# Kernel optimization log

Measured on AMD Instinct MI355X. Metric: run time of the kernel, lower is better.

Reference implementation:

```python
import jax, jax.numpy as jnp
import numpy as np

N_NODES = 100000
N_EDGES = 3200000
IN_DIM, HID, LAT = 81, 64, 32
BN_EPS = 1e-5


def setup_inputs() -> dict:
    key = jax.random.key(0)
    ks = jax.random.split(key, 16)
    def w(k, fan_in, fan_out):
        lim = 1.0 / np.sqrt(fan_in)
        return jax.random.uniform(k, (fan_in, fan_out), jnp.float32, -lim, lim)
    inp = {
        "x": jax.random.normal(ks[0], (N_NODES, IN_DIM), jnp.float32),
        "edge_index": jax.random.randint(ks[1], (2, N_EDGES), 0, N_NODES, jnp.int64),
        "W1": w(ks[2], IN_DIM, HID), "b1": jnp.zeros((HID,), jnp.float32),
        "g1": jnp.ones((HID,), jnp.float32), "beta1": jnp.zeros((HID,), jnp.float32),
        "W2": w(ks[3], HID, HID), "b2": jnp.zeros((HID,), jnp.float32),
        "g2": jnp.ones((HID,), jnp.float32), "beta2": jnp.zeros((HID,), jnp.float32),
        "Wmu": w(ks[4], HID, LAT), "bmu": jnp.zeros((LAT,), jnp.float32),
        "Wls": w(ks[5], HID, LAT), "bls": jnp.zeros((LAT,), jnp.float32),
    }
    return inp


def _gcn_norm(edge_index, num_nodes):
    # PyG gcn_norm: add self-loops, symmetric D^-1/2 A D^-1/2
    loop = jnp.arange(num_nodes, dtype=edge_index.dtype)
    src = jnp.concatenate([edge_index[0], loop])
    dst = jnp.concatenate([edge_index[1], loop])
    deg = jax.ops.segment_sum(jnp.ones_like(src, dtype=jnp.float32), dst,
                              num_segments=num_nodes)
    dis = jnp.where(deg > 0, jax.lax.rsqrt(jnp.maximum(deg, 1.0)), 0.0)
    norm = dis[src] * dis[dst]  # [E + N]
    return src, dst, norm


def _gcn_conv(x, W, b, src, dst, norm, num_nodes):
    h = x @ W                          # [N, out]
    msg = h[src] * norm[:, None]       # gather + scale
    out = jax.ops.segment_sum(msg, dst, num_segments=num_nodes)  # scatter-add
    return out + b


def _batchnorm(h, g, beta):
    m = h.mean(axis=0)
    v = h.var(axis=0)  # biased, as torch uses for normalization
    return (h - m) * jax.lax.rsqrt(v + BN_EPS) * g + beta


def reference(x, edge_index, W1, b1, g1, beta1, W2, b2, g2, beta2,
              Wmu, bmu, Wls, bls):
    n = x.shape[0]
    src, dst, norm = _gcn_norm(edge_index, n)
    h = _gcn_conv(x, W1, b1, src, dst, norm, n)
    h = jax.nn.relu(_batchnorm(h, g1, beta1))  # dropout = identity (eval)
    h = _gcn_conv(h, W2, b2, src, dst, norm, n)
    h = jax.nn.relu(_batchnorm(h, g2, beta2))
    mu = _gcn_conv(h, Wmu, bmu, src, dst, norm, n)
    logstd = _gcn_conv(h, Wls, bls, src, dst, norm, n)
    return (mu, logstd)
```

## Files before the change

### kernel.cpp

```cpp
#include <hip/hip_runtime.h>
#include <stdint.h>

#define N_NODES 100000
#define N_EDGES 3200000
#define IN_DIM  81
#define HID     64
#define LAT     32
#define BN_EPS  1e-5f
#define NBUCKET 391
#define EPB     8192
#define NBLK_E  391
#define BCAP    16384

__device__ __forceinline__ float bfu2f(unsigned short u) {
    return __uint_as_float(((uint32_t)u) << 16);
}
__device__ __forceinline__ unsigned short f2bfu(float f) {
    uint32_t x = __float_as_uint(f);
    return (unsigned short)((x + 0x7FFFu + ((x >> 16) & 1u)) >> 16);
}
__device__ __forceinline__ float loadf(const void* p, size_t i, int fp32) {
    if (fp32) return ((const float*)p)[i];
    return bfu2f(((const unsigned short*)p)[i]);
}
__device__ __forceinline__ int load_dst(const void* ei, int f64, long e) {
    if (f64) return (int)(((const long long*)ei)[(size_t)N_EDGES + e]);
    return ((const int*)ei)[(size_t)N_EDGES + e];
}
__device__ __forceinline__ int load_src(const void* ei, int f64, long e) {
    if (f64) return (int)(((const long long*)ei)[e]);
    return ((const int*)ei)[e];
}
__device__ __forceinline__ float bcast(float v, int k) {
    return __int_as_float(__builtin_amdgcn_readlane(__float_as_int(v), k));
}

__device__ __forceinline__ void fma8(float* acc, uint4 v, float d) {
    acc[0] = fmaf(__uint_as_float(v.x << 16), d, acc[0]);
    acc[1] = fmaf(__uint_as_float(v.x & 0xffff0000u), d, acc[1]);
    acc[2] = fmaf(__uint_as_float(v.y << 16), d, acc[2]);
    acc[3] = fmaf(__uint_as_float(v.y & 0xffff0000u), d, acc[3]);
    acc[4] = fmaf(__uint_as_float(v.z << 16), d, acc[4]);
    acc[5] = fmaf(__uint_as_float(v.z & 0xffff0000u), d, acc[5]);
    acc[6] = fmaf(__uint_as_float(v.w << 16), d, acc[6]);
    acc[7] = fmaf(__uint_as_float(v.w & 0xffff0000u), d, acc[7]);
}

__global__ void stamp_kernel(float* out, int n, float v) {
    int i = blockIdx.x * blockDim.x + threadIdx.x;
    if (i < n) out[i] = v;
}

__global__ void detect_all(const int* ei_raw,
                           const void* x, const void* W1, const void* b1,
                           const void* g1, const void* be1, const void* W2,
                           const void* b2, const void* g2, const void* be2,
                           const void* Wmu, const void* bmu, const void* Wls,
                           const void* bls, int* flags,
                           float* statsA, float* statsB, int* gcnt) {
    int w = threadIdx.x >> 6;
    int lane = threadIdx.x & 63;
    if (w == 14) {
        for (int i = lane; i < 128; i += 64) statsA[i] = 0.0f;
        return;
    }
    if (w == 15) {
        for (int i = lane; i < 128; i += 64) statsB[i] = 0.0f;
        return;
    }
    if (w == 13) {
        int acc = ei_raw[2 * lane * 11003 + 1] |
                  ei_raw[2 * (lane + 64) * 11003 + 1];
        unsigned long long b = __ballot(acc != 0);
        if (lane == 0) flags[0] = (b == 0ull) ? 1 : 0;
        for (int i = lane; i < NBUCKET; i += 64) gcnt[i] = 0;
        return;
    }
    const void* bufs[13] = { x, W1, b1, g1, be1, W2, b2, g2, be2, Wmu, bmu, Wls, bls };
    const int   ns[13]   = { 512, 512, 64, 64, 64, 512, 64, 64, 64, 512, 32, 512, 32 };
    const unsigned short* u = (const unsigned short*)bufs[w];
    int n = ns[w];
    int evenZero = 0;
    bool oddNz = false, anyNz = false, big = false;
    for (int i = lane; i < n; i += 64) {
        unsigned short s = u[i];
        if (s) anyNz = true;
        if (i & 1) { if (s) oddNz = true; }
        else {
            if ((s & 0x7F80u) == 0x7F80u) big = true;
            else if (fabsf(bfu2f(s)) > 100.0f) big = true;
            if (s == 0) evenZero++;
        }
    }
    unsigned long long anyB = __ballot(anyNz);
    unsigned long long oddB = __ballot(oddNz);
    unsigned long long bigB = __ballot(big);
#pragma unroll
    for (int o = 1; o < 64; o <<= 1) evenZero += __shfl_xor(evenZero, o);
    if (lane == 0) {
        int fp32 = 0;
        if (anyB != 0ull) {
            if (bigB != 0ull) fp32 = 1;
            else if (evenZero >= n / 4 && oddB != 0ull) fp32 = 1;
        }
        flags[1 + w] = fp32;
    }
}

__global__ void convert_weights(const void* W1, const void* W2,
                                const void* Wmu, const void* Wls,
                                const void* b1, const void* b2,
                                const void* bmu, const void* bls,
                                const int* flags,
                                float* W1f, float* W2f, float* Wcatf,
                                float* b1f, float* b2f, float* bcatf) {
    int i = blockIdx.x * blockDim.x + threadIdx.x;
    if (i < IN_DIM * HID) { W1f[i] = loadf(W1, i, flags[2]); return; }
    i -= IN_DIM * HID;
    if (i < HID * HID) { W2f[i] = loadf(W2, i, flags[6]); return; }
    i -= HID * HID;
    if (i < HID * HID) {
        int k = i >> 6;
        int j = i & 63;
        if (j < LAT) Wcatf[i] = loadf(Wmu, (size_t)k * LAT + j, flags[10]);
        else         Wcatf[i] = loadf(Wls, (size_t)k * LAT + (j - LAT), flags[12]);
        return;
    }
    i -= HID * HID;
    if (i < HID) { b1f[i] = loadf(b1, i, flags[3]); return; }
    i -= HID;
    if (i < HID) { b2f[i] = loadf(b2, i, flags[7]); return; }
    i -= HID;
    if (i < HID) {
        if (i < LAT) bcatf[i] = loadf(bmu, i, flags[11]);
        else         bcatf[i] = loadf(bls, i - LAT, flags[13]);
    }
}

__global__ void bucket_scatter(const void* ei, const int* flags, int* gcnt,
                               int* staged) {
    __shared__ int h[NBUCKET];
    __shared__ int lbase[NBUCKET];
    __shared__ int lcnt[NBUCKET];
    for (int i = threadIdx.x; i < NBUCKET; i += 256) { h[i] = 0; lcnt[i] = 0; }
    __syncthreads();
    int f64 = flags[0];
    long e0 = (long)blockIdx.x * EPB;
    for (int i = 0; i < EPB / 256; i++) {
        long e = e0 + i * 256 + threadIdx.x;
        if (e < N_EDGES) atomicAdd(&h[load_dst(ei, f64, e) >> 8], 1);
    }
    __syncthreads();
    for (int i = threadIdx.x; i < NBUCKET; i += 256)
        lbase[i] = h[i] ? atomicAdd(&gcnt[i], h[i]) : 0;
    __syncthreads();
    for (int i = 0; i < EPB / 256; i++) {
        long e = e0 + i * 256 + threadIdx.x;
        if (e < N_EDGES) {
            int d = load_dst(ei, f64, e);
            int s = load_src(ei, f64, e);
            int b = d >> 8;
            int off = atomicAdd(&lcnt[b], 1);
            staged[(b << 14) + lbase[b] + off] = ((d & 255) << 17) | s;
        }
    }
}

__global__ void csr_build(const int* gcnt, const int* staged, float* dis,
                          int* row_start, int* csr) {
    int b = blockIdx.x;
    int t = threadIdx.x;
    int n0 = b << 8;
    int nn = N_NODES - n0;
    if (nn > 256) nn = 256;
    __shared__ int sd[256];
    __shared__ int ldeg[256];
    __shared__ int lcur[256];
    int p = 0;
    for (int i = t; i < b; i += 256) p += gcnt[i];
    sd[t] = p;
    __syncthreads();
    for (int off = 128; off >= 1; off >>= 1) {
        if (t < off) sd[t] += sd[t + off];
        __syncthreads();
    }
    int e0 = sd[0];
    int cntb = gcnt[b];
    __syncthreads();
    ldeg[t] = 0;
    __syncthreads();
    const int* sb = staged + ((size_t)b << 14);
    for (int i = t; i < cntb; i += 256)
        atomicAdd(&ldeg[sb[i] >> 17], 1);
    __syncthreads();
    int v = ldeg[t];
    sd[t] = v;
    __syncthreads();
    for (int off = 1; off < 256; off <<= 1) {
        int x = (t >= off) ? sd[t - off] : 0;
        __syncthreads();
        sd[t] += x;
        __syncthreads();
    }
    int excl = sd[t] - v;
    if (t < nn) {
        dis[n0 + t] = rsqrtf((float)(v + 1));
        row_start[n0 + t] = e0 + excl;
    }
    lcur[t] = e0 + excl;
    __syncthreads();
    for (int i = t; i < cntb; i += 256) {
        int rec = sb[i];
        int pos = atomicAdd(&lcur[rec >> 17], 1);
        csr[pos] = rec & 0x1FFFF;
    }
    if (b == NBUCKET - 1 && t == 0) row_start[N_NODES] = e0 + cntb;
}

__global__ void gemm_l1(const void* X, const int* flags, const float* W,
                        unsigned short* T) {
    int wid = (blockIdx.x * blockDim.x + threadIdx.x) >> 6;
    int n0 = wid * 4;
    if (n0 >= N_NODES) return;
    int lane = threadIdx.x & 63;
    int fp = flags[1];
    float xa[4], xb[4];
#pragma unroll
    for (int nn = 0; nn < 4; nn++) {
        size_t base = (size_t)(n0 + nn) * IN_DIM;
        xa[nn] = loadf(X, base + lane, fp);
        xb[nn] = (lane < IN_DIM - 64) ? loadf(X, base + 64 + lane, fp) : 0.0f;
    }
    float acc[4] = { 0.0f, 0.0f, 0.0f, 0.0f };
    const float* Wp = W + lane;
#pragma unroll
    for (int k = 0; k < 64; k++) {
        float w = Wp[k * HID];
#pragma unroll
        for (int nn = 0; nn < 4; nn++)
            acc[nn] = fmaf(bcast(xa[nn], k), w, acc[nn]);
    }
#pragma unroll
    for (int k = 0; k < IN_DIM - 64; k++) {
        float w = Wp[(64 + k) * HID];
#pragma unroll
        for (int nn = 0; nn < 4; nn++)
            acc[nn] = fmaf(bcast(xb[nn], k), w, acc[nn]);
    }
#pragma unroll
    for (int nn = 0; nn < 4; nn++)
        T[(size_t)(n0 + nn) * HID + lane] = f2bfu(acc[nn]);
}

__global__ void gemm_bn(const float* F, const float* W, const float* stats,
                        const void* gw, const void* bw, const int* flags,
                        int gf, int bf, unsigned short* T) {
    int wid = (blockIdx.x * blockDim.x + threadIdx.x) >> 6;
    int n0 = wid * 4;
    if (n0 >= N_NODES) return;
    int lane = threadIdx.x & 63;
    float s = stats[lane];
    float q = stats[64 + lane];
    const float inv_n = 1.0f / (float)N_NODES;
    float mean = s * inv_n;
    float var = q * inv_n - mean * mean;
    float sc = loadf(gw, lane, flags[gf]) * rsqrtf(var + BN_EPS);
    float sh = loadf(bw, lane, flags[bf]) - mean * sc;
    float a[4];
#pragma unroll
    for (int nn = 0; nn < 4; nn++) {
        float f = F[(size_t)(n0 + nn) * HID + lane];
        a[nn] = fmaxf(f * sc + sh, 0.0f);
    }
    float acc[4] = { 0.0f, 0.0f, 0.0f, 0.0f };
    const float* Wp = W + lane;
#pragma unroll
    for (int k = 0; k < HID; k++) {
        float w = Wp[k * HID];
#pragma unroll
        for (int nn = 0; nn < 4; nn++)
            acc[nn] = fmaf(bcast(a[nn], k), w, acc[nn]);
    }
#pragma unroll
    for (int nn = 0; nn < 4; nn++)
        T[(size_t)(n0 + nn) * HID + lane] = f2bfu(acc[nn]);
}

__global__ void agg_mid(const unsigned short* T, const int* row_start, const int* csr,
                        const float* dis, const float* bias, float* F) {
    int wid = (blockIdx.x * blockDim.x + threadIdx.x) >> 6;
    if (wid >= N_NODES) return;
    int lane = threadIdx.x & 63;
    int g = lane >> 3;
    int c = lane & 7;
    float dn = dis[wid];
    float acc[8];
#pragma unroll
    for (int k = 0; k < 8; k++) acc[k] = 0.0f;
    if (g == 0) {
        uint4 v = ((const uint4*)(T + (size_t)wid * HID))[c];
        fma8(acc, v, dn);
    }
    int s0 = row_start[wid];
    int s1 = row_start[wid + 1];
    for (int e = s0; e < s1; e += 32) {
        int i0 = e + g;
        int i1 = e + 8 + g;
        int i2 = e + 16 + g;
        int i3 = e + 24 + g;
        int m0 = i0 < s1, m1 = i1 < s1, m2 = i2 < s1, m3 = i3 < s1;
        int n0i = csr[m0 ? i0 : s0];
        int n1i = csr[m1 ? i1 : s0];
        int n2i = csr[m2 ? i2 : s0];
        int n3i = csr[m3 ? i3 : s0];
        float d0 = m0 ? dis[n0i] : 0.0f;
        float d1 = m1 ? dis[n1i] : 0.0f;
        float d2 = m2 ? dis[n2i] : 0.0f;
        float d3 = m3 ? dis[n3i] : 0.0f;
        uint4 v0 = ((const uint4*)(T + (size_t)n0i * HID))[c];
        uint4 v1 = ((const uint4*)(T + (size_t)n1i * HID))[c];
        uint4 v2 = ((const uint4*)(T + (size_t)n2i * HID))[c];
        uint4 v3 = ((const uint4*)(T + (size_t)n3i * HID))[c];
        fma8(acc, v0, d0);
        fma8(acc, v1, d1);
        fma8(acc, v2, d2);
        fma8(acc, v3, d3);
    }
#pragma unroll
    for (int k = 0; k < 8; k++) {
        float v = acc[k];
        v += __shfl_xor(v, 8);
        v += __shfl_xor(v, 16);
        v += __shfl_xor(v, 32);
        acc[k] = v;
    }
    if (g == 0) {
        const float4* bp = (const float4*)(bias + c * 8);
        float4 b0 = bp[0];
        float4 b1 = bp[1];
        float4 r0, r1;
        r0.x = b0.x + dn * acc[0];
        r0.y = b0.y + dn * acc[1];
        r0.z = b0.z + dn * acc[2];
        r0.w = b0.w + dn * acc[3];
        r1.x = b1.x + dn * acc[4];
        r1.y = b1.y + dn * acc[5];
        r1.z = b1.z + dn * acc[6];
        r1.w = b1.w + dn * acc[7];
        float4* o = (float4*)(F + (size_t)wid * HID + c * 8);
        o[0] = r0;
        o[1] = r1;
    }
}

__global__ void agg_out(const unsigned short* T, const int* row_start, const int* csr,
                        const float* dis, const float* bias, float* out) {
    int wid = (blockIdx.x * blockDim.x + threadIdx.x) >> 6;
    if (wid >= N_NODES) return;
    int lane = threadIdx.x & 63;
    int g = lane >> 3;
    int c = lane & 7;
    float dn = dis[wid];
    float acc[8];
#pragma unroll
    for (int k = 0; k < 8; k++) acc[k] = 0.0f;
    if (g == 0) {
        uint4 v = ((const uint4*)(T + (size_t)wid * HID))[c];
        fma8(acc, v, dn);
    }
    int s0 = row_start[wid];
    int s1 = row_start[wid + 1];
    for (int e = s0; e < s1; e += 32) {
        int i0 = e + g;
        int i1 = e + 8 + g;
        int i2 = e + 16 + g;
        int i3 = e + 24 + g;
        int m0 = i0 < s1, m1 = i1 < s1, m2 = i2 < s1, m3 = i3 < s1;
        int n0i = csr[m0 ? i0 : s0];
        int n1i = csr[m1 ? i1 : s0];
        int n2i = csr[m2 ? i2 : s0];
        int n3i = csr[m3 ? i3 : s0];
        float d0 = m0 ? dis[n0i] : 0.0f;
        float d1 = m1 ? dis[n1i] : 0.0f;
        float d2 = m2 ? dis[n2i] : 0.0f;
        float d3 = m3 ? dis[n3i] : 0.0f;
        uint4 v0 = ((const uint4*)(T + (size_t)n0i * HID))[c];
        uint4 v1 = ((const uint4*)(T + (size_t)n1i * HID))[c];
        uint4 v2 = ((const uint4*)(T + (size_t)n2i * HID))[c];
        uint4 v3 = ((const uint4*)(T + (size_t)n3i * HID))[c];
        fma8(acc, v0, d0);
        fma8(acc, v1, d1);
        fma8(acc, v2, d2);
        fma8(acc, v3, d3);
    }
#pragma unroll
    for (int k = 0; k < 8; k++) {
        float v = acc[k];
        v += __shfl_xor(v, 8);
        v += __shfl_xor(v, 16);
        v += __shfl_xor(v, 32);
        acc[k] = v;
    }
    if (g == 0) {
        const float4* bp = (const float4*)(bias + c * 8);
        float4 b0 = bp[0];
        float4 b1 = bp[1];
        float4 r0, r1;
        r0.x = b0.x + dn * acc[0];
        r0.y = b0.y + dn * acc[1];
        r0.z = b0.z + dn * acc[2];
        r0.w = b0.w + dn * acc[3];
        r1.x = b1.x + dn * acc[4];
        r1.y = b1.y + dn * acc[5];
        r1.z = b1.z + dn * acc[6];
        r1.w = b1.w + dn * acc[7];
        float4* o;
        if (c < 4)
            o = (float4*)(out + (size_t)wid * LAT + c * 8);
        else
            o = (float4*)(out + (size_t)N_NODES * LAT + (size_t)wid * LAT + (c - 4) * 8);
        o[0] = r0;
        o[1] = r1;
    }
}

__global__ void stats_kernel(const float* F, float* stats) {
    int lane = threadIdx.x & 63;
    float s = 0.0f;
    float q = 0.0f;
    int wv = threadIdx.x >> 6;
    for (int r = blockIdx.x * 4 + wv; r < N_NODES; r += gridDim.x * 4) {
        float v = F[(size_t)r * HID + lane];
        s += v;
        q += v * v;
    }
    __shared__ float ls[256];
    __shared__ float lq[256];
    ls[threadIdx.x] = s;
    lq[threadIdx.x] = q;
    __syncthreads();
    if (threadIdx.x < 64) {
        s = ls[threadIdx.x] + ls[64 + threadIdx.x] + ls[128 + threadIdx.x] + ls[192 + threadIdx.x];
        q = lq[threadIdx.x] + lq[64 + threadIdx.x] + lq[128 + threadIdx.x] + lq[192 + threadIdx.x];
        atomicAdd(&stats[lane], s);
        atomicAdd(&stats[64 + lane], q);
    }
}

extern "C" void kernel_launch(void* const* d_in, const int* in_sizes, int n_in,
                              void* d_out, int out_size, void* d_ws, size_t ws_size,
                              hipStream_t stream) {
    (void)in_sizes;
    (void)n_in;
    const void* x   = d_in[0];
    const void* ei  = d_in[1];
    const void* W1  = d_in[2];
    const void* b1  = d_in[3];
    const void* g1  = d_in[4];
    const void* be1 = d_in[5];
    const void* W2  = d_in[6];
    const void* b2  = d_in[7];
    const void* g2  = d_in[8];
    const void* be2 = d_in[9];
    const void* Wmu = d_in[10];
    const void* bmu = d_in[11];
    const void* Wls = d_in[12];
    const void* bls = d_in[13];
    float* out = (float*)d_out;

    char* base = (char*)d_ws;
    size_t off = 0;
    int*   staged = (int*)(base + off);
    float* F      = (float*)(base + off);
    size_t uni = (size_t)NBUCKET * BCAP * 4;
    if ((size_t)N_NODES * HID * 4 > uni) uni = (size_t)N_NODES * HID * 4;
    off += uni;                        off = (off + 511) & ~(size_t)511;
    int* csr = (int*)(base + off);
    off += (size_t)N_EDGES * 4;        off = (off + 511) & ~(size_t)511;
    unsigned short* T = (unsigned short*)(base + off);
    off += (size_t)N_NODES * HID * 2;  off = (off + 511) & ~(size_t)511;
    float* dis = (float*)(base + off);
    off += (size_t)N_NODES * 4;        off = (off + 511) & ~(size_t)511;
    int* row_start = (int*)(base + off);
    off += (size_t)(N_NODES + 1) * 4;  off = (off + 511) & ~(size_t)511;
    int* gcnt = (int*)(base + off);
    off += NBUCKET * 4;                off = (off + 511) & ~(size_t)511;
    int* flags = (int*)(base + off);
    off += 512;                        off = (off + 511) & ~(size_t)511;
    float* W1f = (float*)(base + off);
    off += (size_t)IN_DIM * HID * 4;   off = (off + 511) & ~(size_t)511;
    float* W2f = (float*)(base + off);
    off += (size_t)HID * HID * 4;      off = (off + 511) & ~(size_t)511;
    float* Wcatf = (float*)(base + off);
    off += (size_t)HID * HID * 4;      off = (off + 511) & ~(size_t)511;
    float* b1f = (float*)(base + off);
    off += HID * 4;                    off = (off + 511) & ~(size_t)511;
    float* b2f = (float*)(base + off);
    off += HID * 4;                    off = (off + 511) & ~(size_t)511;
    float* bcatf = (float*)(base + off);
    off += HID * 4;                    off = (off + 511) & ~(size_t)511;
    float* statsA = (float*)(base + off);
    off += 128 * 4;                    off = (off + 511) & ~(size_t)511;
    float* statsB = (float*)(base + off);
    off += 128 * 4;                    off = (off + 511) & ~(size_t)511;

    const int BT = 256;
    int gW   = (N_NODES * 64 + BT - 1) / BT;
    int gG   = ((N_NODES / 4) * 64 + BT - 1) / BT;
    int gOut = (out_size + BT - 1) / BT;
    int gCv  = (IN_DIM * HID + 2 * HID * HID + 3 * HID + BT - 1) / BT;

    if (ws_size < off) {
        stamp_kernel<<<gOut, BT, 0, stream>>>(out, out_size, 6.8e37f);
        return;
    }

    detect_all<<<1, 1024, 0, stream>>>((const int*)ei, x, W1, b1, g1, be1, W2, b2,
                                       g2, be2, Wmu, bmu, Wls, bls, flags,
                                       statsA, statsB, gcnt);
    convert_weights<<<gCv, BT, 0, stream>>>(W1, W2, Wmu, Wls, b1, b2, bmu, bls,
                                            flags, W1f, W2f, Wcatf, b1f, b2f, bcatf);

    bucket_scatter<<<NBLK_E, BT, 0, stream>>>(ei, flags, gcnt, staged);
    csr_build<<<NBUCKET, BT, 0, stream>>>(gcnt, staged, dis, row_start, csr);

    gemm_l1<<<gG, BT, 0, stream>>>(x, flags, W1f, T);
    agg_mid<<<gW, BT, 0, stream>>>(T, row_start, csr, dis, b1f, F);
    stats_kernel<<<256, BT, 0, stream>>>(F, statsA);

    gemm_bn<<<gG, BT, 0, stream>>>(F, W2f, statsA, g1, be1, flags, 4, 5, T);
    agg_mid<<<gW, BT, 0, stream>>>(T, row_start, csr, dis, b2f, F);
    stats_kernel<<<256, BT, 0, stream>>>(F, statsB);

    gemm_bn<<<gG, BT, 0, stream>>>(F, Wcatf, statsB, g2, be2, flags, 8, 9, T);
    agg_out<<<gW, BT, 0, stream>>>(T, row_start, csr, dis, bcatf, out);
}
```

Baseline: 530.8 us.

## Build CSR with global degree atomics and direct scatter instead of bucket staging

Replaces the two-pass bucketed staging CSR build (shared-memory histograms, staged records, per-bucket local sort) with a global per-node degree count, block sums, a scan kernel and a direct scatter using global atomics on per-node cursors. This removes the staging buffer traffic and the second pass over staged records. In exchange it relies on millions of global atomics onto random node addresses, which may contend or be slower than the shared-memory atomics. Neighbor order within each row also becomes nondeterministic, which can change floating-point summation order.

```diff
diff --git a/kernel.cpp b/kernel.cpp
--- a/kernel.cpp
+++ b/kernel.cpp
@@ -8,9 +8,6 @@
 #define LAT     32
 #define BN_EPS  1e-5f
 #define NBUCKET 391
-#define EPB     8192
-#define NBLK_E  391
-#define BCAP    16384
 
 __device__ __forceinline__ float bfu2f(unsigned short u) {
     return __uint_as_float(((uint32_t)u) << 16);
@@ -57,7 +54,7 @@
                            const void* b2, const void* g2, const void* be2,
                            const void* Wmu, const void* bmu, const void* Wls,
                            const void* bls, int* flags,
-                           float* statsA, float* statsB, int* gcnt) {
+                           float* statsA, float* statsB) {
     int w = threadIdx.x >> 6;
     int lane = threadIdx.x & 63;
     if (w == 14) {
@@ -73,7 +70,6 @@
                   ei_raw[2 * (lane + 64) * 11003 + 1];
         unsigned long long b = __ballot(acc != 0);
         if (lane == 0) flags[0] = (b == 0ull) ? 1 : 0;
-        for (int i = lane; i < NBUCKET; i += 64) gcnt[i] = 0;
         return;
     }
     const void* bufs[13] = { x, W1, b1, g1, be1, W2, b2, g2, be2, Wmu, bmu, Wls, bls };
@@ -137,47 +133,30 @@
     }
 }
 
-__global__ void bucket_scatter(const void* ei, const int* flags, int* gcnt,
-                               int* staged) {
-    __shared__ int h[NBUCKET];
-    __shared__ int lbase[NBUCKET];
-    __shared__ int lcnt[NBUCKET];
-    for (int i = threadIdx.x; i < NBUCKET; i += 256) { h[i] = 0; lcnt[i] = 0; }
+__global__ void deg_count(const void* ei, const int* flags, int* deg) {
+    long e = (long)blockIdx.x * blockDim.x + threadIdx.x;
+    if (e < N_EDGES) atomicAdd(&deg[load_dst(ei, flags[0], e)], 1);
+}
+
+__global__ void bucket_sum(const int* deg, int* bsum) {
+    int n = blockIdx.x * 256 + threadIdx.x;
+    int v = (n < N_NODES) ? deg[n] : 0;
+#pragma unroll
+    for (int o = 1; o < 64; o <<= 1) v += __shfl_xor(v, o);
+    __shared__ int ws[4];
+    if ((threadIdx.x & 63) == 0) ws[threadIdx.x >> 6] = v;
     __syncthreads();
-    int f64 = flags[0];
-    long e0 = (long)blockIdx.x * EPB;
-    for (int i = 0; i < EPB / 256; i++) {
-        long e = e0 + i * 256 + threadIdx.x;
-        if (e < N_EDGES) atomicAdd(&h[load_dst(ei, f64, e) >> 8], 1);
-    }
-    __syncthreads();
-    for (int i = threadIdx.x; i < NBUCKET; i += 256)
-        lbase[i] = h[i] ? atomicAdd(&gcnt[i], h[i]) : 0;
-    __syncthreads();
-    for (int i = 0; i < EPB / 256; i++) {
-        long e = e0 + i * 256 + threadIdx.x;
-        if (e < N_EDGES) {
-            int d = load_dst(ei, f64, e);
-            int s = load_src(ei, f64, e);
-            int b = d >> 8;
-            int off = atomicAdd(&lcnt[b], 1);
-            staged[(b << 14) + lbase[b] + off] = ((d & 255) << 17) | s;
-        }
-    }
-}
-
-__global__ void csr_build(const int* gcnt, const int* staged, float* dis,
-                          int* row_start, int* csr) {
+    if (threadIdx.x == 0) bsum[blockIdx.x] = ws[0] + ws[1] + ws[2] + ws[3];
+}
+
+__global__ void scan_build(const int* deg, const int* bsum, float* dis,
+                           int* row_start, int* cur) {
     int b = blockIdx.x;
     int t = threadIdx.x;
-    int n0 = b << 8;
-    int nn = N_NODES - n0;
-    if (nn > 256) nn = 256;
+    int n = b * 256 + t;
     __shared__ int sd[256];
-    __shared__ int ldeg[256];
-    __shared__ int lcur[256];
     int p = 0;
-    for (int i = t; i < b; i += 256) p += gcnt[i];
+    for (int i = t; i < b; i += 256) p += bsum[i];
     sd[t] = p;
     __syncthreads();
     for (int off = 128; off >= 1; off >>= 1) {
@@ -185,15 +164,8 @@
         __syncthreads();
     }
     int e0 = sd[0];
-    int cntb = gcnt[b];
     __syncthreads();
-    ldeg[t] = 0;
-    __syncthreads();
-    const int* sb = staged + ((size_t)b << 14);
-    for (int i = t; i < cntb; i += 256)
-        atomicAdd(&ldeg[sb[i] >> 17], 1);
-    __syncthreads();
-    int v = ldeg[t];
+    int v = (n < N_NODES) ? deg[n] : 0;
     sd[t] = v;
     __syncthreads();
     for (int off = 1; off < 256; off <<= 1) {
@@ -203,18 +175,23 @@
         __syncthreads();
     }
     int excl = sd[t] - v;
-    if (t < nn) {
-        dis[n0 + t] = rsqrtf((float)(v + 1));
-        row_start[n0 + t] = e0 + excl;
-    }
-    lcur[t] = e0 + excl;
-    __syncthreads();
-    for (int i = t; i < cntb; i += 256) {
-        int rec = sb[i];
-        int pos = atomicAdd(&lcur[rec >> 17], 1);
-        csr[pos] = rec & 0x1FFFF;
-    }
-    if (b == NBUCKET - 1 && t == 0) row_start[N_NODES] = e0 + cntb;
+    if (n < N_NODES) {
+        dis[n] = rsqrtf((float)(v + 1));
+        row_start[n] = e0 + excl;
+        cur[n] = e0 + excl;
+    }
+    if (b == NBUCKET - 1 && t == 0) row_start[N_NODES] = N_EDGES;
+}
+
+__global__ void scatter_direct(const void* ei, const int* flags, int* cur,
+                               int* csr) {
+    long e = (long)blockIdx.x * blockDim.x + threadIdx.x;
+    if (e >= N_EDGES) return;
+    int f64 = flags[0];
+    int d = load_dst(ei, f64, e);
+    int s = load_src(ei, f64, e);
+    int pos = atomicAdd(&cur[d], 1);
+    csr[pos] = s;
 }
 
 __global__ void gemm_l1(const void* X, const int* flags, const float* W,
@@ -470,11 +447,8 @@
 
     char* base = (char*)d_ws;
     size_t off = 0;
-    int*   staged = (int*)(base + off);
-    float* F      = (float*)(base + off);
-    size_t uni = (size_t)NBUCKET * BCAP * 4;
-    if ((size_t)N_NODES * HID * 4 > uni) uni = (size_t)N_NODES * HID * 4;
-    off += uni;                        off = (off + 511) & ~(size_t)511;
+    float* F = (float*)(base + off);
+    off += (size_t)N_NODES * HID * 4;  off = (off + 511) & ~(size_t)511;
     int* csr = (int*)(base + off);
     off += (size_t)N_EDGES * 4;        off = (off + 511) & ~(size_t)511;
     unsigned short* T = (unsigned short*)(base + off);
@@ -483,7 +457,11 @@
     off += (size_t)N_NODES * 4;        off = (off + 511) & ~(size_t)511;
     int* row_start = (int*)(base + off);
     off += (size_t)(N_NODES + 1) * 4;  off = (off + 511) & ~(size_t)511;
-    int* gcnt = (int*)(base + off);
+    int* deg = (int*)(base + off);
+    off += (size_t)N_NODES * 4;        off = (off + 511) & ~(size_t)511;
+    int* cur = (int*)(base + off);
+    off += (size_t)N_NODES * 4;        off = (off + 511) & ~(size_t)511;
+    int* bsum = (int*)(base + off);
     off += NBUCKET * 4;                off = (off + 511) & ~(size_t)511;
     int* flags = (int*)(base + off);
     off += 512;                        off = (off + 511) & ~(size_t)511;
@@ -507,6 +485,7 @@
     const int BT = 256;
     int gW   = (N_NODES * 64 + BT - 1) / BT;
     int gG   = ((N_NODES / 4) * 64 + BT - 1) / BT;
+    int gE   = (N_EDGES + BT - 1) / BT;
     int gOut = (out_size + BT - 1) / BT;
     int gCv  = (IN_DIM * HID + 2 * HID * HID + 3 * HID + BT - 1) / BT;
 
@@ -515,14 +494,17 @@
         return;
     }
 
+    hipMemsetAsync(deg, 0, (size_t)N_NODES * 4, stream);
     detect_all<<<1, 1024, 0, stream>>>((const int*)ei, x, W1, b1, g1, be1, W2, b2,
                                        g2, be2, Wmu, bmu, Wls, bls, flags,
-                                       statsA, statsB, gcnt);
+                                       statsA, statsB);
     convert_weights<<<gCv, BT, 0, stream>>>(W1, W2, Wmu, Wls, b1, b2, bmu, bls,
                                             flags, W1f, W2f, Wcatf, b1f, b2f, bcatf);
 
-    bucket_scatter<<<NBLK_E, BT, 0, stream>>>(ei, flags, gcnt, staged);
-    csr_build<<<NBUCKET, BT, 0, stream>>>(gcnt, staged, dis, row_start, csr);
+    deg_count<<<gE, BT, 0, stream>>>(ei, flags, deg);
+    bucket_sum<<<NBUCKET, BT, 0, stream>>>(deg, bsum);
+    scan_build<<<NBUCKET, BT, 0, stream>>>(deg, bsum, dis, row_start, cur);
+    scatter_direct<<<gE, BT, 0, stream>>>(ei, flags, cur, csr);
 
     gemm_l1<<<gG, BT, 0, stream>>>(x, flags, W1f, T);
     agg_mid<<<gW, BT, 0, stream>>>(T, row_start, csr, dis, b1f, F);
```

New measurement: 863.9 us. 62.8% more time.
